# Performance work log

Hardware: AMD Instinct MI355X
Metric: run time of the kernel (lower is better)

Reference implementation:

```python
import jax, jax.numpy as jnp
import numpy as np

N, D, O, V, E, C = 100000, 128, 128, 3, 400000, 2

def setup_inputs() -> dict:
    key = jax.random.key(0)
    ks = jax.random.split(key, 32)
    s = 0.05
    inp = {
        'features': jax.random.normal(ks[0], (N, D), jnp.float32),
        'edge_index': jax.random.randint(ks[1], (V, 2, E), 0, N, jnp.int32),
        'edge_weight': jax.random.uniform(ks[2], (V, E), jnp.float32),
        # per-view RelationAggregator (single relation each)
        'rel_w': jax.random.normal(ks[3], (V, D, O)) * s,
        'rel_b': jnp.zeros((V, O)),
        'gate_w': jax.random.normal(ks[4], (V, O, O)) * s,
        'gate_b': jnp.zeros((V, O)),
        # LabelAwareAttention
        'la_w1': jax.random.normal(ks[5], (C, D, D // 2)) * s,
        'la_b1': jnp.zeros((C, D // 2)),
        'la_w2': jax.random.normal(ks[6], (C, D // 2)) * s,
        'la_b2': jnp.zeros((C,)),
        'pred_w': jax.random.normal(ks[7], (D, C)) * s,
        'pred_b': jnp.zeros((C,)),
        'att_bias': jnp.float32(0.1),
        # ViewLevelAttention
        'view_pref': jax.random.normal(ks[8], (V, O)),
        'va_w1': jax.random.normal(ks[9], (O, O // 2)) * s,
        'va_b1': jnp.zeros((O // 2,)),
        'va_w2': jax.random.normal(ks[10], (O // 2,)) * s,
        'va_b2': jnp.float32(0.0),
        # linear heads
        'ft_w': jax.random.normal(ks[11], (D, O)) * s,
        'ft_b': jnp.zeros((O,)),
        'sl_w': jax.random.normal(ks[12], (D, O)) * s,
        'sl_b': jnp.zeros((O,)),
        'fus_w': jax.random.normal(ks[13], (2 * O, O)) * s,
        'fus_b': jnp.zeros((O,)),
        'ln_g': jnp.ones((O,)),
        'ln_beta': jnp.zeros((O,)),
    }
    return inp


def _aggregate_view(features, ei, ew, w, b, gw, gb):
    # gather -> linear -> edge weight -> scatter-add (fused segment_sum)
    msg = (features[ei[0]] @ w + b) * ew[:, None]          # [E, O]
    agg = jax.ops.segment_sum(msg, ei[1], num_segments=N)  # [N, O]
    # relation_weight_net: softmax over 1 relation == 1.0 (identity)
    gate = jax.nn.sigmoid(agg @ gw + gb)
    return gate * agg


def reference(features, edge_index, edge_weight, rel_w, rel_b, gate_w, gate_b,
              la_w1, la_b1, la_w2, la_b2, pred_w, pred_b, att_bias,
              view_pref, va_w1, va_b1, va_w2, va_b2,
              ft_w, ft_b, sl_w, sl_b, fus_w, fus_b, ln_g, ln_beta):
    # --- label-aware attention ---
    class_probs = jax.nn.softmax(features @ pred_w + pred_b, axis=-1)        # [N, C]
    h = jax.nn.relu(jnp.einsum('nd,cdk->nck', features, la_w1) + la_b1)      # [N, C, D/2]
    scores = jax.nn.sigmoid(jnp.einsum('nck,ck->nc', h, la_w2) + la_b2)      # [N, C]
    node_att = jnp.sum(scores * class_probs, axis=-1) + att_bias             # [N]

    # --- per-view relation aggregation ---
    views = jax.vmap(_aggregate_view, in_axes=(None, 0, 0, 0, 0, 0, 0))(
        features, edge_index, edge_weight, rel_w, rel_b, gate_w, gate_b)     # [V, N, O]

    # --- view-level attention ---
    pe = views * view_pref[:, None, :]                                       # [V, N, O]
    vh = jax.nn.relu(jnp.einsum('vno,ok->vnk', pe, va_w1) + va_b1)           # [V, N, O/2]
    vscore = jnp.einsum('vnk,k->vn', vh, va_w2) + va_b2                      # [V, N]
    v_att = jax.nn.softmax(vscore, axis=0)                                   # over views
    combined = jnp.sum(views * v_att[..., None], axis=0)                     # [N, O]

    # --- fusion (dropout in eval mode == identity) ---
    self_out = features @ sl_w + sl_b
    transformed = features @ ft_w + ft_b
    weighted = combined * node_att[:, None]
    fused = jax.nn.relu(jnp.concatenate([self_out, weighted], axis=-1) @ fus_w + fus_b)
    out = fused + transformed

    mu = jnp.mean(out, axis=-1, keepdims=True)
    var = jnp.mean(jnp.square(out - mu), axis=-1, keepdims=True)
    out = (out - mu) / jnp.sqrt(var + 1e-5) * ln_g + ln_beta
    return out, class_probs
```

## Files before the change

### kernel.cpp

```cpp
#include <hip/hip_runtime.h>

#define N_ 100000
#define D_ 128
#define O_ 128
#define V_ 3
#define E_ 400000
#define NB_SCAN 98
#define EGRID 1563
#define MB 32
#define NBLK (N_ / MB)
#define LDA 136

#define PRE_CVT  6250
#define PRE_PREW (PRE_CVT + 64)
#define PRE_PREP (PRE_PREW + 683)
#define PRE_TOT  (PRE_PREP + 3 * EGRID)

typedef unsigned short u16;
typedef __attribute__((ext_vector_type(8))) short bf16x8;
typedef __attribute__((ext_vector_type(4))) float f32x4;

#define MFMA16x16x32 __builtin_amdgcn_mfma_f32_16x16x32_bf16

#define P_RELB  0
#define P_GATEB 384
#define P_VP    768
#define P_VAB1  1152
#define P_VAW2  1216
#define P_VAB2  1280
#define P_LAB1  1281
#define P_LAW2  1409
#define P_LAB2  1537
#define P_PREDB 1539
#define P_ATTB  1541
#define P_FTB   1542
#define P_LNG   1670
#define P_LNB   1798
#define P_PREDW 1926
#define P_TOTAL 2182

__device__ __forceinline__ float b2f(u16 u) {
    union { float f; unsigned int i; } x; x.i = ((unsigned int)u) << 16; return x.f;
}
__device__ __forceinline__ float blo(unsigned int u) {
    union { float f; unsigned int i; } x; x.i = u << 16; return x.f;
}
__device__ __forceinline__ float bhi(unsigned int u) {
    union { float f; unsigned int i; } x; x.i = u & 0xffff0000u; return x.f;
}
__device__ __forceinline__ u16 f2b(float f) {
    union { float f; unsigned int i; } x; x.f = f;
    unsigned int r = x.i + 0x7FFFu + ((x.i >> 16) & 1u);
    return (u16)(r >> 16);
}

template<int F32> __device__ __forceinline__ float LD(const void* p, size_t i) {
    if (F32) return ((const float*)p)[i];
    return b2f(((const u16*)p)[i]);
}

__global__ void k_detect(const u16* __restrict__ feat, int* __restrict__ flag) {
    int t = threadIdx.x;
    u16 a = feat[2 * t], b = feat[2 * t + 128];
    int zeros = (a == 0 ? 1 : 0) + (b == 0 ? 1 : 0);
    float va = b2f(a), vb = b2f(b);
    int bad = (!(va > -128.f && va < 128.f) ? 1 : 0) +
              (!(vb > -128.f && vb < 128.f) ? 1 : 0);
    #pragma unroll
    for (int s = 1; s <= 32; s <<= 1) {
        bad += __shfl_xor(bad, s);
        zeros += __shfl_xor(zeros, s);
    }
    if (t == 0) flag[0] = (bad >= 16 || zeros >= 64) ? 1 : 0;
}

__device__ __forceinline__ void cvt_body_f32(int b, const void* feat,
                                             u16* __restrict__ featB) {
    size_t idx = (size_t)b * 256 + threadIdx.x;
    const float4* fp = (const float4*)feat;
    float4 a = fp[idx * 2], c = fp[idx * 2 + 1];
    uint4 u;
    u.x = (unsigned)f2b(a.x) | ((unsigned)f2b(a.y) << 16);
    u.y = (unsigned)f2b(a.z) | ((unsigned)f2b(a.w) << 16);
    u.z = (unsigned)f2b(c.x) | ((unsigned)f2b(c.y) << 16);
    u.w = (unsigned)f2b(c.z) | ((unsigned)f2b(c.w) << 16);
    ((uint4*)featB)[idx] = u;
}

template<int F32>
__device__ __forceinline__ void prew_body(int b, const void* sl_w, const void* sl_b,
                                          const void* fus_w, const void* fus_b,
                                          u16* __restrict__ W1T, float* __restrict__ b1) {
    int gid = b * 256 + threadIdx.x;
    int d = gid >> 7, o = gid & 127;
    float acc = 0.f;
    for (int k = 0; k < 128; ++k)
        acc += LD<F32>(sl_w, d * 128 + k) * LD<F32>(fus_w, k * 128 + o);
    W1T[o * 128 + d] = f2b(acc);
    if (gid < 128) {
        float accb = 0.f;
        for (int k = 0; k < 128; ++k)
            accb += LD<F32>(sl_b, k) * LD<F32>(fus_w, k * 128 + gid);
        b1[gid] = accb + LD<F32>(fus_b, gid);
    }
}

template<int F32>
__device__ __forceinline__ void prep_body(int b,
        const void* rel_w, const void* gate_w, const void* va_w1, const void* fus_w,
        const void* ft_w, const void* la_w1,
        const void* rel_b, const void* gate_b, const void* vpref,
        const void* va_b1, const void* va_w2, const void* va_b2,
        const void* la_b1, const void* la_w2, const void* la_b2,
        const void* pred_b, const void* att_bias, const void* ft_b,
        const void* ln_g, const void* ln_beta, const void* pred_w,
        u16* __restrict__ relT, u16* __restrict__ rgT, u16* __restrict__ vaT3,
        u16* __restrict__ fus2T, u16* __restrict__ ftT, u16* __restrict__ laT,
        float* __restrict__ P, float* __restrict__ rgb) {
    int id = b * 256 + threadIdx.x;
    if (id < 49152) {
        int v = id >> 14, r = id & 16383, o = r >> 7, d = r & 127;
        relT[id] = f2b(LD<F32>(rel_w, (size_t)v * 16384 + d * 128 + o));
    } else if (id < 73728) {
        int t = id - 49152, v = t >> 13, r = t & 8191, n = r >> 7, k = r & 127;
        vaT3[t] = f2b(LD<F32>(va_w1, k * 64 + n) * LD<F32>(vpref, v * 128 + k));
    } else if (id < 90112) {
        int t = id - 73728, n = t >> 7, k = t & 127;
        fus2T[t] = f2b(LD<F32>(fus_w, (128 + k) * 128 + n));
    } else if (id < 106496) {
        int t = id - 90112, o = t >> 7, d = t & 127;
        ftT[t] = f2b(LD<F32>(ft_w, d * 128 + o));
    } else if (id < 122880) {
        int t = id - 106496, n = t >> 7, d = t & 127;
        int c = n >> 6, j = n & 63;
        laT[t] = f2b(LD<F32>(la_w1, c * 8192 + d * 64 + j));
    } else if (id < 122880 + P_TOTAL) {
        int t = id - 122880;
        float val;
        if      (t < P_GATEB) val = LD<F32>(rel_b, t);
        else if (t < P_VP)    val = LD<F32>(gate_b, t - P_GATEB);
        else if (t < P_VAB1)  val = LD<F32>(vpref, t - P_VP);
        else if (t < P_VAW2)  val = LD<F32>(va_b1, t - P_VAB1);
        else if (t < P_VAB2)  val = LD<F32>(va_w2, t - P_VAW2);
        else if (t < P_LAB1)  val = LD<F32>(va_b2, 0);
        else if (t < P_LAW2)  val = LD<F32>(la_b1, t - P_LAB1);
        else if (t < P_LAB2)  val = LD<F32>(la_w2, t - P_LAW2);
        else if (t < P_PREDB) val = LD<F32>(la_b2, t - P_LAB2);
        else if (t < P_ATTB)  val = LD<F32>(pred_b, t - P_PREDB);
        else if (t < P_FTB)   val = LD<F32>(att_bias, 0);
        else if (t < P_LNG)   val = LD<F32>(ft_b, t - P_FTB);
        else if (t < P_LNB)   val = LD<F32>(ln_g, t - P_LNG);
        else if (t < P_PREDW) val = LD<F32>(ln_beta, t - P_LNB);
        else                  val = LD<F32>(pred_w, t - P_PREDW);
        P[t] = val;
    } else if (id < 174214) {
        int t = id - 125062, v = t >> 14, r = t & 16383, n = r >> 7, d = r & 127;
        float acc = 0.f;
        for (int o = 0; o < 128; ++o)
            acc += LD<F32>(rel_w,  (size_t)v * 16384 + d * 128 + o) *
                   LD<F32>(gate_w, (size_t)v * 16384 + o * 128 + n);
        rgT[t] = f2b(acc);
    } else if (id < 174598) {
        int t = id - 174214, v = t >> 7, n = t & 127;
        float acc = 0.f;
        for (int o = 0; o < 128; ++o)
            acc += LD<F32>(rel_b, v * 128 + o) *
                   LD<F32>(gate_w, (size_t)v * 16384 + o * 128 + n);
        rgb[t] = acc;
    }
}

__global__ __launch_bounds__(256) void k_preC(const int* __restrict__ flag,
        const void* feat, u16* __restrict__ featB,
        const void* sl_w, const void* sl_b, const void* fus_w, const void* fus_b,
        u16* __restrict__ W1T, float* __restrict__ b1,
        const void* rel_w, const void* gate_w, const void* va_w1,
        const void* ft_w, const void* la_w1,
        const void* rel_b, const void* gate_b, const void* vpref,
        const void* va_b1, const void* va_w2, const void* va_b2,
        const void* la_b1, const void* la_w2, const void* la_b2,
        const void* pred_b, const void* att_bias, const void* ft_b,
        const void* ln_g, const void* ln_beta, const void* pred_w,
        u16* __restrict__ relT, u16* __restrict__ rgT, u16* __restrict__ vaT3,
        u16* __restrict__ fus2T, u16* __restrict__ ftT, u16* __restrict__ laT,
        float* __restrict__ P, float* __restrict__ rgb,
        const int* __restrict__ ei, int* __restrict__ cur3) {
    int b = blockIdx.x;
    if (b < PRE_CVT) {
        if (flag[0]) cvt_body_f32(b, feat, featB);
    } else if (b < PRE_PREW) {
        if (flag[0]) prew_body<1>(b - PRE_CVT, sl_w, sl_b, fus_w, fus_b, W1T, b1);
        else         prew_body<0>(b - PRE_CVT, sl_w, sl_b, fus_w, fus_b, W1T, b1);
    } else if (b < PRE_PREP) {
        if (flag[0]) prep_body<1>(b - PRE_PREW, rel_w, gate_w, va_w1, fus_w, ft_w, la_w1,
                                  rel_b, gate_b, vpref, va_b1, va_w2, va_b2,
                                  la_b1, la_w2, la_b2, pred_b, att_bias, ft_b,
                                  ln_g, ln_beta, pred_w, relT, rgT, vaT3, fus2T, ftT, laT, P, rgb);
        else         prep_body<0>(b - PRE_PREW, rel_w, gate_w, va_w1, fus_w, ft_w, la_w1,
                                  rel_b, gate_b, vpref, va_b1, va_w2, va_b2,
                                  la_b1, la_w2, la_b2, pred_b, att_bias, ft_b,
                                  ln_g, ln_beta, pred_w, relT, rgT, vaT3, fus2T, ftT, laT, P, rgb);
    } else {
        int b2 = b - PRE_PREP;
        int v = b2 / EGRID;
        int e = (b2 % EGRID) * 256 + threadIdx.x;
        if (e < E_) atomicAdd(&cur3[v * N_ + ei[(size_t)v * 2 * E_ + E_ + e]], 1);
    }
}

__global__ __launch_bounds__(256) void k_scan_bsum(const int* __restrict__ cur3,
                                                   int* __restrict__ bsum) {
    __shared__ int red[256];
    const int v = blockIdx.x / NB_SCAN, b = blockIdx.x % NB_SCAN, tid = threadIdx.x;
    const int base = b * 1024;
    const int* counts = cur3 + v * N_;
    int s = 0;
    for (int i = tid; i < 1024; i += 256) {
        int idx = base + i;
        s += (idx < N_) ? counts[idx] : 0;
    }
    red[tid] = s;
    __syncthreads();
    for (int st = 128; st >= 1; st >>= 1) {
        if (tid < st) red[tid] += red[tid + st];
        __syncthreads();
    }
    if (tid == 0) bsum[v * 128 + b] = red[0];
}

__global__ __launch_bounds__(256) void k_scan_write(int* __restrict__ cur3,
                                                    const int* __restrict__ bsum,
                                                    int* __restrict__ offs3) {
    __shared__ int lsum[256];
    __shared__ int bs_s[128];
    const int v = blockIdx.x / NB_SCAN, b = blockIdx.x % NB_SCAN, tid = threadIdx.x;
    const int base = b * 1024;
    int* counts = cur3 + v * N_;
    int* offs   = offs3 + v * N_;
    if (tid < 128) bs_s[tid] = (tid < b) ? bsum[v * 128 + tid] : 0;
    int c[4]; int s = 0;
    #pragma unroll
    for (int k = 0; k < 4; ++k) {
        int idx = base + tid * 4 + k;
        c[k] = (idx < N_) ? counts[idx] : 0;
        s += c[k];
    }
    lsum[tid] = s;
    __syncthreads();
    for (int st = 1; st < 256; st <<= 1) {
        int t = (tid >= st) ? lsum[tid - st] : 0;
        __syncthreads();
        lsum[tid] += t;
        __syncthreads();
    }
    for (int st = 64; st >= 1; st >>= 1) {
        if (tid < st) bs_s[tid] += bs_s[tid + st];
        __syncthreads();
    }
    int off = bs_s[0] + lsum[tid] - s;
    #pragma unroll
    for (int k = 0; k < 4; ++k) {
        int idx = base + tid * 4 + k;
        if (idx < N_) { offs[idx] = off; counts[idx] = off; }
        off += c[k];
    }
}

template<int F32>
__device__ __forceinline__ void place_body(const int* __restrict__ ei, const void* ew_all,
                                           int* __restrict__ cur3, int2* __restrict__ srcw3) {
    int v = blockIdx.x / EGRID;
    int e = (blockIdx.x % EGRID) * 256 + threadIdx.x;
    if (e < E_) {
        int dst = ei[(size_t)v * 2 * E_ + E_ + e];
        int src = ei[(size_t)v * 2 * E_ + e];
        float w = LD<F32>(ew_all, (size_t)v * E_ + e);
        int pos = atomicAdd(&cur3[v * N_ + dst], 1);
        int2 sw; sw.x = src; sw.y = __float_as_int(w);
        srcw3[(size_t)v * E_ + pos] = sw;
    }
}
__global__ __launch_bounds__(256) void k_place(const int* __restrict__ flag,
                                               const int* __restrict__ ei, const void* ew,
                                               int* __restrict__ cur3, int2* __restrict__ srcw3) {
    if (flag[0]) place_body<1>(ei, ew, cur3, srcw3);
    else         place_body<0>(ei, ew, cur3, srcw3);
}

__global__ __launch_bounds__(768, 6) void k_fused(const int* __restrict__ flag,
        const void* feat, const u16* __restrict__ featB_,
        const int2* __restrict__ srcw3,
        const int* __restrict__ offs3, const int* __restrict__ ends3,
        const u16* __restrict__ relT, const u16* __restrict__ rgT,
        const u16* __restrict__ vaT3, const u16* __restrict__ W1T,
        const u16* __restrict__ fus2T, const u16* __restrict__ ftT,
        const u16* __restrict__ laT,
        const float* __restrict__ b1, const float* __restrict__ rgb,
        const float* __restrict__ P,
        void* __restrict__ d_out) {
    const int f32 = flag[0];
    const u16* __restrict__ fb = f32 ? featB_ : (const u16*)feat;

    __shared__ __align__(16) u16 S[4 * MB * LDA];
    __shared__ float redL[4][MB];
    __shared__ float redv[3][4][MB];
    __shared__ float wsn3[3][MB];
    __shared__ float aw_s[MB][3];
    __shared__ float natt_s[MB];
    __shared__ float lg_s[MB][2];
    __shared__ float mrs_s[MB][2];

    u16* xA = S;
    float* F1 = (float*)(S + 2 * MB * LDA);
    float* F2 = (float*)S;
    float* red2 = &redv[0][0][0];

    const int tid = threadIdx.x;
    const int g   = tid >> 8;
    const int t256 = tid & 255;
    const int wid = t256 >> 6;
    const int L = t256 & 63, q = L >> 4, i = L & 15;
    const int nb = wid * 32;
    const int nodebase = blockIdx.x * MB;
    const int nl = t256 >> 5, l32 = t256 & 31, o4 = l32 * 4;
    const int gsub = t256 >> 4, l16 = tid & 15, o8 = l16 * 8;
    const f32x4 zz = {0.f, 0.f, 0.f, 0.f};
    u16* zc = S + (size_t)(1 + g) * MB * LDA;

    auto ldf = [&](const u16* B, int row, int k0) -> bf16x8 {
        return *(const bf16x8*)&B[row * LDA + k0];
    };
    auto ldg = [&](const u16* B, int row, int k0) -> bf16x8 {
        return *(const bf16x8*)&B[row * 128 + k0];
    };
    auto gemm32 = [&](const u16* A, const u16* Bg, f32x4 acc[2][2]) {
        #pragma unroll
        for (int kk = 0; kk < 4; ++kk) {
            int k0 = q * 8 + kk * 32;
            bf16x8 a0 = ldf(A, i, k0);
            bf16x8 a1 = ldf(A, i + 16, k0);
            bf16x8 bb0 = ldg(Bg, nb + i, k0);
            bf16x8 bb1 = ldg(Bg, nb + 16 + i, k0);
            acc[0][0] = MFMA16x16x32(a0, bb0, acc[0][0], 0, 0, 0);
            acc[0][1] = MFMA16x16x32(a0, bb1, acc[0][1], 0, 0, 0);
            acc[1][0] = MFMA16x16x32(a1, bb0, acc[1][0], 0, 0, 0);
            acc[1][1] = MFMA16x16x32(a1, bb1, acc[1][1], 0, 0, 0);
        }
    };
    auto gemm32x2 = [&](const u16* A, const u16* B0g, const u16* B1g,
                        f32x4 accA[2][2], f32x4 accB[2][2]) {
        #pragma unroll
        for (int kk = 0; kk < 4; ++kk) {
            int k0 = q * 8 + kk * 32;
            bf16x8 a0 = ldf(A, i, k0);
            bf16x8 a1 = ldf(A, i + 16, k0);
            bf16x8 p0 = ldg(B0g, nb + i, k0);
            bf16x8 p1 = ldg(B0g, nb + 16 + i, k0);
            bf16x8 r0 = ldg(B1g, nb + i, k0);
            bf16x8 r1 = ldg(B1g, nb + 16 + i, k0);
            accA[0][0] = MFMA16x16x32(a0, p0, accA[0][0], 0, 0, 0);
            accA[0][1] = MFMA16x16x32(a0, p1, accA[0][1], 0, 0, 0);
            accA[1][0] = MFMA16x16x32(a1, p0, accA[1][0], 0, 0, 0);
            accA[1][1] = MFMA16x16x32(a1, p1, accA[1][1], 0, 0, 0);
            accB[0][0] = MFMA16x16x32(a0, r0, accB[0][0], 0, 0, 0);
            accB[0][1] = MFMA16x16x32(a0, r1, accB[0][1], 0, 0, 0);
            accB[1][0] = MFMA16x16x32(a1, r0, accB[1][0], 0, 0, 0);
            accB[1][1] = MFMA16x16x32(a1, r1, accB[1][1], 0, 0, 0);
        }
    };
    auto gather = [&]() {
        const int* offs = offs3 + g * N_;
        const int* ends = ends3 + g * N_;
        const int2* srcw = srcw3 + (size_t)g * E_;
        #pragma unroll
        for (int rep = 0; rep < 2; ++rep) {
            const int m = gsub + rep * 16;
            const int node = nodebase + m;
            float z0 = 0.f, z1 = 0.f, z2 = 0.f, z3 = 0.f;
            float z4 = 0.f, z5 = 0.f, z6 = 0.f, z7 = 0.f, ws = 0.f;
            int j = offs[node], jend = ends[node];
            while (j < jend) {
                int r = jend - j;
                int2 e0 = srcw[j];
                int2 e1, e2, e3;
                e1.x = 0; e1.y = 0; e2.x = 0; e2.y = 0; e3.x = 0; e3.y = 0;
                if (r > 1) e1 = srcw[j + 1];
                if (r > 2) e2 = srcw[j + 2];
                if (r > 3) e3 = srcw[j + 3];
                uint4 x0, x1, x2, x3;
                x1.x = x1.y = x1.z = x1.w = 0;
                x2.x = x2.y = x2.z = x2.w = 0;
                x3.x = x3.y = x3.z = x3.w = 0;
                x0 = *(const uint4*)&fb[(size_t)e0.x * 128 + o8];
                if (r > 1) x1 = *(const uint4*)&fb[(size_t)e1.x * 128 + o8];
                if (r > 2) x2 = *(const uint4*)&fb[(size_t)e2.x * 128 + o8];
                if (r > 3) x3 = *(const uint4*)&fb[(size_t)e3.x * 128 + o8];
                float w0 = __int_as_float(e0.y), w1 = __int_as_float(e1.y);
                float w2 = __int_as_float(e2.y), w3 = __int_as_float(e3.y);
                ws += w0 + w1 + w2 + w3;
                z0 += w0 * blo(x0.x) + w1 * blo(x1.x) + w2 * blo(x2.x) + w3 * blo(x3.x);
                z1 += w0 * bhi(x0.x) + w1 * bhi(x1.x) + w2 * bhi(x2.x) + w3 * bhi(x3.x);
                z2 += w0 * blo(x0.y) + w1 * blo(x1.y) + w2 * blo(x2.y) + w3 * blo(x3.y);
                z3 += w0 * bhi(x0.y) + w1 * bhi(x1.y) + w2 * bhi(x2.y) + w3 * bhi(x3.y);
                z4 += w0 * blo(x0.z) + w1 * blo(x1.z) + w2 * blo(x2.z) + w3 * blo(x3.z);
                z5 += w0 * bhi(x0.z) + w1 * bhi(x1.z) + w2 * bhi(x2.z) + w3 * bhi(x3.z);
                z6 += w0 * blo(x0.w) + w1 * blo(x1.w) + w2 * blo(x2.w) + w3 * blo(x3.w);
                z7 += w0 * bhi(x0.w) + w1 * bhi(x1.w) + w2 * bhi(x2.w) + w3 * bhi(x3.w);
                j += 4;
            }
            uint4 u;
            u.x = (unsigned)f2b(z0) | ((unsigned)f2b(z1) << 16);
            u.y = (unsigned)f2b(z2) | ((unsigned)f2b(z3) << 16);
            u.z = (unsigned)f2b(z4) | ((unsigned)f2b(z5) << 16);
            u.w = (unsigned)f2b(z6) | ((unsigned)f2b(z7) << 16);
            *(uint4*)&zc[m * LDA + o8] = u;
            if (l16 == 0) wsn3[g][m] = ws;
        }
    };

    if (tid < 512) {
        int m = tid >> 4, s = tid & 15;
        *(uint4*)&xA[m * LDA + s * 8] =
            *(const uint4*)&fb[(size_t)(nodebase + m) * 128 + s * 8];
    }
    gather();
    __syncthreads();

    if (g == 1) {
        f32x4 accL[2][2] = {{zz, zz}, {zz, zz}};
        gemm32(xA, laT, accL);
        float la0 = P[P_LAB1 + nb + i],  la1 = P[P_LAB1 + nb + 16 + i];
        float lw0 = P[P_LAW2 + nb + i],  lw1 = P[P_LAW2 + nb + 16 + i];
        float partL[2][4];
        #pragma unroll
        for (int mt = 0; mt < 2; ++mt)
            #pragma unroll
            for (int r = 0; r < 4; ++r) {
                float h0 = fmaxf(accL[mt][0][r] + la0, 0.f);
                float h1 = fmaxf(accL[mt][1][r] + la1, 0.f);
                partL[mt][r] = h0 * lw0 + h1 * lw1;
            }
        #pragma unroll
        for (int s = 1; s <= 8; s <<= 1)
            #pragma unroll
            for (int mt = 0; mt < 2; ++mt)
                #pragma unroll
                for (int r = 0; r < 4; ++r)
                    partL[mt][r] += __shfl_xor(partL[mt][r], s);
        if (i == 0)
            #pragma unroll
            for (int mt = 0; mt < 2; ++mt)
                #pragma unroll
                for (int r = 0; r < 4; ++r)
                    redL[wid][mt * 16 + q * 4 + r] = partL[mt][r];
    }
    if (g == 2) {
        float pw[8];
        #pragma unroll
        for (int t = 0; t < 4; ++t) {
            pw[2 * t]     = P[P_PREDW + (o4 + t) * 2];
            pw[2 * t + 1] = P[P_PREDW + (o4 + t) * 2 + 1];
        }
        #pragma unroll
        for (int rep = 0; rep < 4; ++rep) {
            int m = rep * 8 + nl;
            float lg0 = 0.f, lg1 = 0.f;
            #pragma unroll
            for (int t = 0; t < 4; ++t) {
                float xv = b2f(xA[m * LDA + o4 + t]);
                lg0 += xv * pw[2 * t];
                lg1 += xv * pw[2 * t + 1];
            }
            #pragma unroll
            for (int s = 1; s <= 16; s <<= 1) {
                lg0 += __shfl_xor(lg0, s);
                lg1 += __shfl_xor(lg1, s);
            }
            if (l32 == 0) { lg_s[m][0] = lg0; lg_s[m][1] = lg1; }
        }
    }
    f32x4 accA[2][2] = {{zz, zz}, {zz, zz}};
    f32x4 accG[2][2] = {{zz, zz}, {zz, zz}};
    gemm32x2(zc, relT + (size_t)g * 16384, rgT + (size_t)g * 16384, accA, accG);
    __syncthreads();

    {
        float rb0 = P[P_RELB + g * 128 + nb + i];
        float rb1 = P[P_RELB + g * 128 + nb + 16 + i];
        float rg0 = rgb[g * 128 + nb + i];
        float rg1 = rgb[g * 128 + nb + 16 + i];
        float gb0 = P[P_GATEB + g * 128 + nb + i];
        float gb1 = P[P_GATEB + g * 128 + nb + 16 + i];
        #pragma unroll
        for (int mt = 0; mt < 2; ++mt)
            #pragma unroll
            for (int nt = 0; nt < 2; ++nt) {
                float rb = nt ? rb1 : rb0;
                float rg = nt ? rg1 : rg0;
                float gb = nt ? gb1 : gb0;
                int col = nb + nt * 16 + i;
                #pragma unroll
                for (int r = 0; r < 4; ++r) {
                    int row = mt * 16 + q * 4 + r;
                    float ws = wsn3[g][row];
                    float agg = accA[mt][nt][r] + ws * rb;
                    float gin = accG[mt][nt][r] + ws * rg + gb;
                    float gt = 1.f / (1.f + __expf(-gin));
                    zc[row * LDA + col] = f2b(gt * agg);
                }
            }
    }
    if (tid < MB) {
        float c0 = redL[0][tid] + redL[1][tid] + P[P_LAB2 + 0];
        float c1 = redL[2][tid] + redL[3][tid] + P[P_LAB2 + 1];
        float s0 = 1.f / (1.f + __expf(-c0));
        float s1 = 1.f / (1.f + __expf(-c1));
        float l0 = lg_s[tid][0] + P[P_PREDB + 0];
        float l1 = lg_s[tid][1] + P[P_PREDB + 1];
        float mx = fmaxf(l0, l1);
        float e0 = __expf(l0 - mx), e1 = __expf(l1 - mx);
        float inv = 1.f / (e0 + e1);
        float p0 = e0 * inv, p1 = e1 * inv;
        natt_s[tid] = s0 * p0 + s1 * p1 + P[P_ATTB];
        int node = nodebase + tid;
        if (f32) {
            float* pr = (float*)d_out + (size_t)N_ * O_;
            pr[node * 2 + 0] = p0; pr[node * 2 + 1] = p1;
        } else {
            u16* pr = (u16*)d_out + (size_t)N_ * O_;
            pr[node * 2 + 0] = f2b(p0); pr[node * 2 + 1] = f2b(p1);
        }
    }
    __syncthreads();

    {
        f32x4 accV[2] = {zz, zz};
        const int nbv = wid * 16, colv = nbv + i;
        const u16* vaW = vaT3 + (size_t)g * 8192;
        #pragma unroll
        for (int kk = 0; kk < 4; ++kk) {
            int k0 = q * 8 + kk * 32;
            bf16x8 bb = ldg(vaW, nbv + i, k0);
            bf16x8 a0 = ldf(zc, i, k0);
            bf16x8 a1 = ldf(zc, i + 16, k0);
            accV[0] = MFMA16x16x32(a0, bb, accV[0], 0, 0, 0);
            accV[1] = MFMA16x16x32(a1, bb, accV[1], 0, 0, 0);
        }
        float vb1v = P[P_VAB1 + colv], vw2v = P[P_VAW2 + colv];
        float part[2][4];
        #pragma unroll
        for (int mt = 0; mt < 2; ++mt)
            #pragma unroll
            for (int r = 0; r < 4; ++r) {
                float vh = fmaxf(accV[mt][r] + vb1v, 0.f);
                part[mt][r] = vh * vw2v;
            }
        #pragma unroll
        for (int s = 1; s <= 8; s <<= 1)
            #pragma unroll
            for (int mt = 0; mt < 2; ++mt)
                #pragma unroll
                for (int r = 0; r < 4; ++r)
                    part[mt][r] += __shfl_xor(part[mt][r], s);
        if (i == 0)
            #pragma unroll
            for (int mt = 0; mt < 2; ++mt)
                #pragma unroll
                for (int r = 0; r < 4; ++r)
                    redv[g][wid][mt * 16 + q * 4 + r] = part[mt][r];
    }
    __syncthreads();

    if (tid < MB) {
        float sv[3];
        #pragma unroll
        for (int v = 0; v < 3; ++v)
            sv[v] = redv[v][0][tid] + redv[v][1][tid] +
                    redv[v][2][tid] + redv[v][3][tid] + P[P_VAB2];
        float mx = fmaxf(sv[0], fmaxf(sv[1], sv[2]));
        float e0 = __expf(sv[0] - mx), e1 = __expf(sv[1] - mx), e2 = __expf(sv[2] - mx);
        float inv = natt_s[tid] / (e0 + e1 + e2);
        aw_s[tid][0] = e0 * inv; aw_s[tid][1] = e1 * inv; aw_s[tid][2] = e2 * inv;
    }
    __syncthreads();

    {
        u16* z0p = S + MB * LDA;
        u16* z1p = S + 2 * MB * LDA;
        u16* z2p = S + 3 * MB * LDA;
        for (int idx = tid; idx < MB * 128; idx += 768) {
            int row = idx >> 7, col = idx & 127;
            float w = aw_s[row][0] * b2f(z0p[row * LDA + col]) +
                      aw_s[row][1] * b2f(z1p[row * LDA + col]) +
                      aw_s[row][2] * b2f(z2p[row * LDA + col]);
            z0p[row * LDA + col] = f2b(w);
        }
    }
    __syncthreads();

    f32x4 accF[2][2] = {{zz, zz}, {zz, zz}};
    if (g == 0) {
        gemm32(xA, W1T, accF);
        #pragma unroll
        for (int mt = 0; mt < 2; ++mt)
            #pragma unroll
            for (int nt = 0; nt < 2; ++nt)
                #pragma unroll
                for (int r = 0; r < 4; ++r)
                    F1[(mt * 16 + q * 4 + r) * 128 + nb + nt * 16 + i] = accF[mt][nt][r];
    } else if (g == 1) {
        gemm32(S + MB * LDA, fus2T, accF);
    } else {
        gemm32(xA, ftT, accF);
    }
    __syncthreads();
    if (g == 1) {
        #pragma unroll
        for (int mt = 0; mt < 2; ++mt)
            #pragma unroll
            for (int nt = 0; nt < 2; ++nt)
                #pragma unroll
                for (int r = 0; r < 4; ++r)
                    F2[(mt * 16 + q * 4 + r) * 128 + nb + nt * 16 + i] = accF[mt][nt][r];
    }
    __syncthreads();

    if (g == 2) {
        float b1v0 = b1[nb + i], b1v1 = b1[nb + 16 + i];
        float fb0 = P[P_FTB + nb + i], fb1 = P[P_FTB + nb + 16 + i];
        float ps[2][4], pq[2][4];
        #pragma unroll
        for (int mt = 0; mt < 2; ++mt)
            #pragma unroll
            for (int r = 0; r < 4; ++r) { ps[mt][r] = 0.f; pq[mt][r] = 0.f; }
        #pragma unroll
        for (int mt = 0; mt < 2; ++mt)
            #pragma unroll
            for (int nt = 0; nt < 2; ++nt) {
                int col = nb + nt * 16 + i;
                float bv = nt ? b1v1 : b1v0;
                float fv = nt ? fb1 : fb0;
                #pragma unroll
                for (int r = 0; r < 4; ++r) {
                    int rc = (mt * 16 + q * 4 + r) * 128 + col;
                    float o = fmaxf(F1[rc] + F2[rc] + bv, 0.f) + accF[mt][nt][r] + fv;
                    F1[rc] = o;
                    ps[mt][r] += o; pq[mt][r] += o * o;
                }
            }
        #pragma unroll
        for (int s = 1; s <= 8; s <<= 1)
            #pragma unroll
            for (int mt = 0; mt < 2; ++mt)
                #pragma unroll
                for (int r = 0; r < 4; ++r) {
                    ps[mt][r] += __shfl_xor(ps[mt][r], s);
                    pq[mt][r] += __shfl_xor(pq[mt][r], s);
                }
        if (i == 0)
            #pragma unroll
            for (int mt = 0; mt < 2; ++mt)
                #pragma unroll
                for (int r = 0; r < 4; ++r) {
                    int row = mt * 16 + q * 4 + r;
                    red2[(wid * MB + row) * 2 + 0] = ps[mt][r];
                    red2[(wid * MB + row) * 2 + 1] = pq[mt][r];
                }
    }
    __syncthreads();

    if (tid < MB) {
        float sm = red2[tid * 2]            + red2[(MB + tid) * 2] +
                   red2[(2 * MB + tid) * 2] + red2[(3 * MB + tid) * 2];
        float sq = red2[tid * 2 + 1]            + red2[(MB + tid) * 2 + 1] +
                   red2[(2 * MB + tid) * 2 + 1] + red2[(3 * MB + tid) * 2 + 1];
        float mu = sm * (1.f / 128.f);
        float var = sq * (1.f / 128.f) - mu * mu;
        mrs_s[tid][0] = mu; mrs_s[tid][1] = rsqrtf(var + 1e-5f);
    }
    __syncthreads();

    if (f32) {
        float* op = (float*)d_out + (size_t)nodebase * 128;
        for (int idx = tid; idx < MB * 128; idx += 768) {
            int row = idx >> 7, col = idx & 127;
            op[idx] = (F1[idx] - mrs_s[row][0]) * mrs_s[row][1]
                      * P[P_LNG + col] + P[P_LNB + col];
        }
    } else {
        unsigned* op = (unsigned*)d_out + (size_t)nodebase * 64;
        for (int idx = tid; idx < MB * 64; idx += 768) {
            int row = idx >> 6, c2 = (idx & 63) * 2;
            float m0 = mrs_s[row][0], r0 = mrs_s[row][1];
            float v0 = (F1[row * 128 + c2]     - m0) * r0 * P[P_LNG + c2]     + P[P_LNB + c2];
            float v1 = (F1[row * 128 + c2 + 1] - m0) * r0 * P[P_LNG + c2 + 1] + P[P_LNB + c2 + 1];
            op[idx] = (unsigned)f2b(v0) | ((unsigned)f2b(v1) << 16);
        }
    }
}

extern "C" void kernel_launch(void* const* d_in, const int* in_sizes, int n_in,
                              void* d_out, int out_size, void* d_ws, size_t ws_size,
                              hipStream_t stream) {
    const void* feat     = d_in[0];
    const int*  ei       = (const int*)d_in[1];
    const void* ew       = d_in[2];
    const void* rel_w    = d_in[3];
    const void* rel_b    = d_in[4];
    const void* gate_w   = d_in[5];
    const void* gate_b   = d_in[6];
    const void* la_w1    = d_in[7];
    const void* la_b1    = d_in[8];
    const void* la_w2    = d_in[9];
    const void* la_b2    = d_in[10];
    const void* pred_w   = d_in[11];
    const void* pred_b   = d_in[12];
    const void* att_bias = d_in[13];
    const void* view_pref= d_in[14];
    const void* va_w1    = d_in[15];
    const void* va_b1    = d_in[16];
    const void* va_w2    = d_in[17];
    const void* va_b2    = d_in[18];
    const void* ft_w     = d_in[19];
    const void* ft_b     = d_in[20];
    const void* sl_w     = d_in[21];
    const void* sl_b     = d_in[22];
    const void* fus_w    = d_in[23];
    const void* fus_b    = d_in[24];
    const void* ln_g     = d_in[25];
    const void* ln_beta  = d_in[26];

    int*   flag  = (int*)d_ws;
    int*   offs3 = flag + 4;
    int*   cur3  = offs3 + 3 * N_;
    int2*  srcw3 = (int2*)(cur3 + 3 * N_);
    int*   bsum  = (int*)(srcw3 + 3 * E_);
    float* b1    = (float*)(bsum + 3 * 128);
    float* P     = b1 + 128;
    float* rgb   = P + 2304;
    u16*   W1T   = (u16*)(rgb + 384);
    u16*   relT  = W1T + 16384;
    u16*   rgT   = relT + 3 * 16384;
    u16*   vaT3  = rgT + 3 * 16384;
    u16*   fus2T = vaT3 + 3 * 8192;
    u16*   ftT   = fus2T + 16384;
    u16*   laT   = ftT + 16384;
    u16*   featB = laT + 16384;

    k_detect<<<1, 64, 0, stream>>>((const u16*)feat, flag);
    (void)hipMemsetAsync(cur3, 0, 3 * N_ * sizeof(int), stream);
    k_preC<<<PRE_TOT, 256, 0, stream>>>(flag, feat, featB,
                                        sl_w, sl_b, fus_w, fus_b, W1T, b1,
                                        rel_w, gate_w, va_w1, ft_w, la_w1,
                                        rel_b, gate_b, view_pref,
                                        va_b1, va_w2, va_b2,
                                        la_b1, la_w2, la_b2,
                                        pred_b, att_bias, ft_b, ln_g, ln_beta, pred_w,
                                        relT, rgT, vaT3, fus2T, ftT, laT, P, rgb,
                                        ei, cur3);
    k_scan_bsum<<<3 * NB_SCAN, 256, 0, stream>>>(cur3, bsum);
    k_scan_write<<<3 * NB_SCAN, 256, 0, stream>>>(cur3, bsum, offs3);
    k_place<<<3 * EGRID, 256, 0, stream>>>(flag, ei, ew, cur3, srcw3);
    k_fused<<<NBLK, 768, 0, stream>>>(flag, feat, featB, srcw3, offs3, cur3,
                                      relT, rgT, vaT3, W1T, fus2T, ftT, laT,
                                      b1, rgb, P, d_out);
}
```

Measured before the change: 517.5 us.

## Inline dtype detection per kernel, drop barriers, and raise MFMA wave priority

Removes the separate single-block detect kernel and instead has each kernel infer the input dtype from the feature bits in every wavefront, cutting one launch and the flag dependency. In the fused kernel, the per-row attention weights and layernorm statistics are now recomputed inline by every thread, which removes two __syncthreads and the shared staging arrays at the cost of redundant exp and reduction arithmetic. MFMA loops are wrapped in s_setprio to favour matrix waves. Every wave now performs extra global reads and shuffles for detection.

```diff
diff --git a/kernel.cpp b/kernel.cpp
--- a/kernel.cpp
+++ b/kernel.cpp
@@ -59,9 +59,10 @@
     return b2f(((const u16*)p)[i]);
 }
 
-__global__ void k_detect(const u16* __restrict__ feat, int* __restrict__ flag) {
-    int t = threadIdx.x;
-    u16 a = feat[2 * t], b = feat[2 * t + 128];
+__device__ __forceinline__ int detect_f32(const void* feat) {
+    const u16* f = (const u16*)feat;
+    int l = threadIdx.x & 63;
+    u16 a = f[2 * l], b = f[2 * l + 128];
     int zeros = (a == 0 ? 1 : 0) + (b == 0 ? 1 : 0);
     float va = b2f(a), vb = b2f(b);
     int bad = (!(va > -128.f && va < 128.f) ? 1 : 0) +
@@ -71,7 +72,7 @@
         bad += __shfl_xor(bad, s);
         zeros += __shfl_xor(zeros, s);
     }
-    if (t == 0) flag[0] = (bad >= 16 || zeros >= 64) ? 1 : 0;
+    return (bad >= 16 || zeros >= 64) ? 1 : 0;
 }
 
 __device__ __forceinline__ void cvt_body_f32(int b, const void* feat,
@@ -170,7 +171,7 @@
     }
 }
 
-__global__ __launch_bounds__(256) void k_preC(const int* __restrict__ flag,
+__global__ __launch_bounds__(256) void k_preC(
         const void* feat, u16* __restrict__ featB,
         const void* sl_w, const void* sl_b, const void* fus_w, const void* fus_b,
         u16* __restrict__ W1T, float* __restrict__ b1,
@@ -185,21 +186,22 @@
         u16* __restrict__ fus2T, u16* __restrict__ ftT, u16* __restrict__ laT,
         float* __restrict__ P, float* __restrict__ rgb,
         const int* __restrict__ ei, int* __restrict__ cur3) {
+    const int f32 = detect_f32(feat);
     int b = blockIdx.x;
     if (b < PRE_CVT) {
-        if (flag[0]) cvt_body_f32(b, feat, featB);
+        if (f32) cvt_body_f32(b, feat, featB);
     } else if (b < PRE_PREW) {
-        if (flag[0]) prew_body<1>(b - PRE_CVT, sl_w, sl_b, fus_w, fus_b, W1T, b1);
-        else         prew_body<0>(b - PRE_CVT, sl_w, sl_b, fus_w, fus_b, W1T, b1);
+        if (f32) prew_body<1>(b - PRE_CVT, sl_w, sl_b, fus_w, fus_b, W1T, b1);
+        else     prew_body<0>(b - PRE_CVT, sl_w, sl_b, fus_w, fus_b, W1T, b1);
     } else if (b < PRE_PREP) {
-        if (flag[0]) prep_body<1>(b - PRE_PREW, rel_w, gate_w, va_w1, fus_w, ft_w, la_w1,
-                                  rel_b, gate_b, vpref, va_b1, va_w2, va_b2,
-                                  la_b1, la_w2, la_b2, pred_b, att_bias, ft_b,
-                                  ln_g, ln_beta, pred_w, relT, rgT, vaT3, fus2T, ftT, laT, P, rgb);
-        else         prep_body<0>(b - PRE_PREW, rel_w, gate_w, va_w1, fus_w, ft_w, la_w1,
-                                  rel_b, gate_b, vpref, va_b1, va_w2, va_b2,
-                                  la_b1, la_w2, la_b2, pred_b, att_bias, ft_b,
-                                  ln_g, ln_beta, pred_w, relT, rgT, vaT3, fus2T, ftT, laT, P, rgb);
+        if (f32) prep_body<1>(b - PRE_PREW, rel_w, gate_w, va_w1, fus_w, ft_w, la_w1,
+                              rel_b, gate_b, vpref, va_b1, va_w2, va_b2,
+                              la_b1, la_w2, la_b2, pred_b, att_bias, ft_b,
+                              ln_g, ln_beta, pred_w, relT, rgT, vaT3, fus2T, ftT, laT, P, rgb);
+        else     prep_body<0>(b - PRE_PREW, rel_w, gate_w, va_w1, fus_w, ft_w, la_w1,
+                              rel_b, gate_b, vpref, va_b1, va_w2, va_b2,
+                              la_b1, la_w2, la_b2, pred_b, att_bias, ft_b,
+                              ln_g, ln_beta, pred_w, relT, rgT, vaT3, fus2T, ftT, laT, P, rgb);
     } else {
         int b2 = b - PRE_PREP;
         int v = b2 / EGRID;
@@ -280,14 +282,14 @@
         srcw3[(size_t)v * E_ + pos] = sw;
     }
 }
-__global__ __launch_bounds__(256) void k_place(const int* __restrict__ flag,
+__global__ __launch_bounds__(256) void k_place(const void* feat,
                                                const int* __restrict__ ei, const void* ew,
                                                int* __restrict__ cur3, int2* __restrict__ srcw3) {
-    if (flag[0]) place_body<1>(ei, ew, cur3, srcw3);
-    else         place_body<0>(ei, ew, cur3, srcw3);
-}
-
-__global__ __launch_bounds__(768, 6) void k_fused(const int* __restrict__ flag,
+    if (detect_f32(feat)) place_body<1>(ei, ew, cur3, srcw3);
+    else                  place_body<0>(ei, ew, cur3, srcw3);
+}
+
+__global__ __launch_bounds__(768, 6) void k_fused(
         const void* feat, const u16* __restrict__ featB_,
         const int2* __restrict__ srcw3,
         const int* __restrict__ offs3, const int* __restrict__ ends3,
@@ -298,17 +300,14 @@
         const float* __restrict__ b1, const float* __restrict__ rgb,
         const float* __restrict__ P,
         void* __restrict__ d_out) {
-    const int f32 = flag[0];
+    const int f32 = detect_f32(feat);
     const u16* __restrict__ fb = f32 ? featB_ : (const u16*)feat;
 
     __shared__ __align__(16) u16 S[4 * MB * LDA];
     __shared__ float redL[4][MB];
     __shared__ float redv[3][4][MB];
     __shared__ float wsn3[3][MB];
-    __shared__ float aw_s[MB][3];
-    __shared__ float natt_s[MB];
     __shared__ float lg_s[MB][2];
-    __shared__ float mrs_s[MB][2];
 
     u16* xA = S;
     float* F1 = (float*)(S + 2 * MB * LDA);
@@ -334,6 +333,7 @@
         return *(const bf16x8*)&B[row * 128 + k0];
     };
     auto gemm32 = [&](const u16* A, const u16* Bg, f32x4 acc[2][2]) {
+        __builtin_amdgcn_s_setprio(1);
         #pragma unroll
         for (int kk = 0; kk < 4; ++kk) {
             int k0 = q * 8 + kk * 32;
@@ -346,9 +346,11 @@
             acc[1][0] = MFMA16x16x32(a1, bb0, acc[1][0], 0, 0, 0);
             acc[1][1] = MFMA16x16x32(a1, bb1, acc[1][1], 0, 0, 0);
         }
+        __builtin_amdgcn_s_setprio(0);
     };
     auto gemm32x2 = [&](const u16* A, const u16* B0g, const u16* B1g,
                         f32x4 accA[2][2], f32x4 accB[2][2]) {
+        __builtin_amdgcn_s_setprio(1);
         #pragma unroll
         for (int kk = 0; kk < 4; ++kk) {
             int k0 = q * 8 + kk * 32;
@@ -367,6 +369,7 @@
             accB[1][0] = MFMA16x16x32(a1, r0, accB[1][0], 0, 0, 0);
             accB[1][1] = MFMA16x16x32(a1, r1, accB[1][1], 0, 0, 0);
         }
+        __builtin_amdgcn_s_setprio(0);
     };
     auto gather = [&]() {
         const int* offs = offs3 + g * N_;
@@ -511,17 +514,12 @@
             }
     }
     if (tid < MB) {
-        float c0 = redL[0][tid] + redL[1][tid] + P[P_LAB2 + 0];
-        float c1 = redL[2][tid] + redL[3][tid] + P[P_LAB2 + 1];
-        float s0 = 1.f / (1.f + __expf(-c0));
-        float s1 = 1.f / (1.f + __expf(-c1));
         float l0 = lg_s[tid][0] + P[P_PREDB + 0];
         float l1 = lg_s[tid][1] + P[P_PREDB + 1];
         float mx = fmaxf(l0, l1);
         float e0 = __expf(l0 - mx), e1 = __expf(l1 - mx);
         float inv = 1.f / (e0 + e1);
         float p0 = e0 * inv, p1 = e1 * inv;
-        natt_s[tid] = s0 * p0 + s1 * p1 + P[P_ATTB];
         int node = nodebase + tid;
         if (f32) {
             float* pr = (float*)d_out + (size_t)N_ * O_;
@@ -537,6 +535,7 @@
         f32x4 accV[2] = {zz, zz};
         const int nbv = wid * 16, colv = nbv + i;
         const u16* vaW = vaT3 + (size_t)g * 8192;
+        __builtin_amdgcn_s_setprio(1);
         #pragma unroll
         for (int kk = 0; kk < 4; ++kk) {
             int k0 = q * 8 + kk * 32;
@@ -546,6 +545,7 @@
             accV[0] = MFMA16x16x32(a0, bb, accV[0], 0, 0, 0);
             accV[1] = MFMA16x16x32(a1, bb, accV[1], 0, 0, 0);
         }
+        __builtin_amdgcn_s_setprio(0);
         float vb1v = P[P_VAB1 + colv], vw2v = P[P_VAW2 + colv];
         float part[2][4];
         #pragma unroll
@@ -571,28 +571,33 @@
     }
     __syncthreads();
 
-    if (tid < MB) {
-        float sv[3];
-        #pragma unroll
-        for (int v = 0; v < 3; ++v)
-            sv[v] = redv[v][0][tid] + redv[v][1][tid] +
-                    redv[v][2][tid] + redv[v][3][tid] + P[P_VAB2];
-        float mx = fmaxf(sv[0], fmaxf(sv[1], sv[2]));
-        float e0 = __expf(sv[0] - mx), e1 = __expf(sv[1] - mx), e2 = __expf(sv[2] - mx);
-        float inv = natt_s[tid] / (e0 + e1 + e2);
-        aw_s[tid][0] = e0 * inv; aw_s[tid][1] = e1 * inv; aw_s[tid][2] = e2 * inv;
-    }
-    __syncthreads();
-
     {
         u16* z0p = S + MB * LDA;
         u16* z1p = S + 2 * MB * LDA;
         u16* z2p = S + 3 * MB * LDA;
+        float vab2 = P[P_VAB2], attb = P[P_ATTB];
+        float lab20 = P[P_LAB2 + 0], lab21 = P[P_LAB2 + 1];
+        float pb0 = P[P_PREDB + 0], pb1 = P[P_PREDB + 1];
         for (int idx = tid; idx < MB * 128; idx += 768) {
             int row = idx >> 7, col = idx & 127;
-            float w = aw_s[row][0] * b2f(z0p[row * LDA + col]) +
-                      aw_s[row][1] * b2f(z1p[row * LDA + col]) +
-                      aw_s[row][2] * b2f(z2p[row * LDA + col]);
+            float c0 = redL[0][row] + redL[1][row] + lab20;
+            float c1 = redL[2][row] + redL[3][row] + lab21;
+            float s0 = 1.f / (1.f + __expf(-c0));
+            float s1 = 1.f / (1.f + __expf(-c1));
+            float l0 = lg_s[row][0] + pb0;
+            float l1 = lg_s[row][1] + pb1;
+            float mx2 = fmaxf(l0, l1);
+            float q0 = __expf(l0 - mx2), q1 = __expf(l1 - mx2);
+            float natt = (s0 * q0 + s1 * q1) / (q0 + q1) + attb;
+            float sv0 = redv[0][0][row] + redv[0][1][row] + redv[0][2][row] + redv[0][3][row] + vab2;
+            float sv1 = redv[1][0][row] + redv[1][1][row] + redv[1][2][row] + redv[1][3][row] + vab2;
+            float sv2 = redv[2][0][row] + redv[2][1][row] + redv[2][2][row] + redv[2][3][row] + vab2;
+            float mx = fmaxf(sv0, fmaxf(sv1, sv2));
+            float e0 = __expf(sv0 - mx), e1 = __expf(sv1 - mx), e2 = __expf(sv2 - mx);
+            float inv = natt / (e0 + e1 + e2);
+            float w = (e0 * b2f(z0p[row * LDA + col]) +
+                       e1 * b2f(z1p[row * LDA + col]) +
+                       e2 * b2f(z2p[row * LDA + col])) * inv;
             z0p[row * LDA + col] = f2b(w);
         }
     }
@@ -669,31 +674,30 @@
     }
     __syncthreads();
 
-    if (tid < MB) {
-        float sm = red2[tid * 2]            + red2[(MB + tid) * 2] +
-                   red2[(2 * MB + tid) * 2] + red2[(3 * MB + tid) * 2];
-        float sq = red2[tid * 2 + 1]            + red2[(MB + tid) * 2 + 1] +
-                   red2[(2 * MB + tid) * 2 + 1] + red2[(3 * MB + tid) * 2 + 1];
-        float mu = sm * (1.f / 128.f);
-        float var = sq * (1.f / 128.f) - mu * mu;
-        mrs_s[tid][0] = mu; mrs_s[tid][1] = rsqrtf(var + 1e-5f);
-    }
-    __syncthreads();
-
     if (f32) {
         float* op = (float*)d_out + (size_t)nodebase * 128;
         for (int idx = tid; idx < MB * 128; idx += 768) {
             int row = idx >> 7, col = idx & 127;
-            op[idx] = (F1[idx] - mrs_s[row][0]) * mrs_s[row][1]
-                      * P[P_LNG + col] + P[P_LNB + col];
+            float sm = red2[row * 2]              + red2[(MB + row) * 2] +
+                       red2[(2 * MB + row) * 2]   + red2[(3 * MB + row) * 2];
+            float sq = red2[row * 2 + 1]            + red2[(MB + row) * 2 + 1] +
+                       red2[(2 * MB + row) * 2 + 1] + red2[(3 * MB + row) * 2 + 1];
+            float mu = sm * (1.f / 128.f);
+            float rs = rsqrtf(sq * (1.f / 128.f) - mu * mu + 1e-5f);
+            op[idx] = (F1[idx] - mu) * rs * P[P_LNG + col] + P[P_LNB + col];
         }
     } else {
         unsigned* op = (unsigned*)d_out + (size_t)nodebase * 64;
         for (int idx = tid; idx < MB * 64; idx += 768) {
             int row = idx >> 6, c2 = (idx & 63) * 2;
-            float m0 = mrs_s[row][0], r0 = mrs_s[row][1];
-            float v0 = (F1[row * 128 + c2]     - m0) * r0 * P[P_LNG + c2]     + P[P_LNB + c2];
-            float v1 = (F1[row * 128 + c2 + 1] - m0) * r0 * P[P_LNG + c2 + 1] + P[P_LNB + c2 + 1];
+            float sm = red2[row * 2]              + red2[(MB + row) * 2] +
+                       red2[(2 * MB + row) * 2]   + red2[(3 * MB + row) * 2];
+            float sq = red2[row * 2 + 1]            + red2[(MB + row) * 2 + 1] +
+                       red2[(2 * MB + row) * 2 + 1] + red2[(3 * MB + row) * 2 + 1];
+            float mu = sm * (1.f / 128.f);
+            float rs = rsqrtf(sq * (1.f / 128.f) - mu * mu + 1e-5f);
+            float v0 = (F1[row * 128 + c2]     - mu) * rs * P[P_LNG + c2]     + P[P_LNB + c2];
+            float v1 = (F1[row * 128 + c2 + 1] - mu) * rs * P[P_LNG + c2 + 1] + P[P_LNB + c2 + 1];
             op[idx] = (unsigned)f2b(v0) | ((unsigned)f2b(v1) << 16);
         }
     }
@@ -747,9 +751,8 @@
     u16*   laT   = ftT + 16384;
     u16*   featB = laT + 16384;
 
-    k_detect<<<1, 64, 0, stream>>>((const u16*)feat, flag);
     (void)hipMemsetAsync(cur3, 0, 3 * N_ * sizeof(int), stream);
-    k_preC<<<PRE_TOT, 256, 0, stream>>>(flag, feat, featB,
+    k_preC<<<PRE_TOT, 256, 0, stream>>>(feat, featB,
                                         sl_w, sl_b, fus_w, fus_b, W1T, b1,
                                         rel_w, gate_w, va_w1, ft_w, la_w1,
                                         rel_b, gate_b, view_pref,
@@ -760,8 +763,8 @@
                                         ei, cur3);
     k_scan_bsum<<<3 * NB_SCAN, 256, 0, stream>>>(cur3, bsum);
     k_scan_write<<<3 * NB_SCAN, 256, 0, stream>>>(cur3, bsum, offs3);
-    k_place<<<3 * EGRID, 256, 0, stream>>>(flag, ei, ew, cur3, srcw3);
-    k_fused<<<NBLK, 768, 0, stream>>>(flag, feat, featB, srcw3, offs3, cur3,
+    k_place<<<3 * EGRID, 256, 0, stream>>>(feat, ei, ew, cur3, srcw3);
+    k_fused<<<NBLK, 768, 0, stream>>>(feat, featB, srcw3, offs3, cur3,
                                       relT, rgT, vaT3, W1T, fus2T, ftT, laT,
                                       b1, rgb, P, d_out);
 }
```

Result: slower. 571.6 us (+10.4%).

## Merge scan kernels, derive CSR starts from counts, drop a fused-kernel barrier

Applied to the files above, without the earlier changes.

Replaces the two-pass block-sum scan with a single kernel where each block sums all preceding counts directly, which removes one launch and the bsum buffer. The placement atomics now advance offs3 in place, so offs3 ends up holding each segment's end and the count array stays intact. The gather derives each segment's start as end minus count. In the fused kernel, the fus2 GEMM result goes into a dedicated shared buffer, which removes one __syncthreads and the extra write phase at the cost of 16KB more LDS per block. That extra LDS may lower occupancy, and the redundant prefix reads grow quadratically with the number of blocks.

```diff
diff --git a/kernel.cpp b/kernel.cpp
--- a/kernel.cpp
+++ b/kernel.cpp
@@ -208,36 +208,24 @@
     }
 }
 
-__global__ __launch_bounds__(256) void k_scan_bsum(const int* __restrict__ cur3,
-                                                   int* __restrict__ bsum) {
+__global__ __launch_bounds__(256) void k_scan_write(const int* __restrict__ cur3,
+                                                    int* __restrict__ offs3) {
     __shared__ int red[256];
+    __shared__ int lsum[256];
+    __shared__ int bs;
     const int v = blockIdx.x / NB_SCAN, b = blockIdx.x % NB_SCAN, tid = threadIdx.x;
     const int base = b * 1024;
     const int* counts = cur3 + v * N_;
-    int s = 0;
-    for (int i = tid; i < 1024; i += 256) {
-        int idx = base + i;
-        s += (idx < N_) ? counts[idx] : 0;
-    }
-    red[tid] = s;
+    int* offs = offs3 + v * N_;
+    int pre = 0;
+    for (int idx = tid; idx < base; idx += 256) pre += counts[idx];
+    red[tid] = pre;
     __syncthreads();
     for (int st = 128; st >= 1; st >>= 1) {
         if (tid < st) red[tid] += red[tid + st];
         __syncthreads();
     }
-    if (tid == 0) bsum[v * 128 + b] = red[0];
-}
-
-__global__ __launch_bounds__(256) void k_scan_write(int* __restrict__ cur3,
-                                                    const int* __restrict__ bsum,
-                                                    int* __restrict__ offs3) {
-    __shared__ int lsum[256];
-    __shared__ int bs_s[128];
-    const int v = blockIdx.x / NB_SCAN, b = blockIdx.x % NB_SCAN, tid = threadIdx.x;
-    const int base = b * 1024;
-    int* counts = cur3 + v * N_;
-    int* offs   = offs3 + v * N_;
-    if (tid < 128) bs_s[tid] = (tid < b) ? bsum[v * 128 + tid] : 0;
+    if (tid == 0) bs = red[0];
     int c[4]; int s = 0;
     #pragma unroll
     for (int k = 0; k < 4; ++k) {
@@ -253,44 +241,40 @@
         lsum[tid] += t;
         __syncthreads();
     }
-    for (int st = 64; st >= 1; st >>= 1) {
-        if (tid < st) bs_s[tid] += bs_s[tid + st];
-        __syncthreads();
-    }
-    int off = bs_s[0] + lsum[tid] - s;
+    int off = bs + lsum[tid] - s;
     #pragma unroll
     for (int k = 0; k < 4; ++k) {
         int idx = base + tid * 4 + k;
-        if (idx < N_) { offs[idx] = off; counts[idx] = off; }
+        if (idx < N_) offs[idx] = off;
         off += c[k];
     }
 }
 
 template<int F32>
 __device__ __forceinline__ void place_body(const int* __restrict__ ei, const void* ew_all,
-                                           int* __restrict__ cur3, int2* __restrict__ srcw3) {
+                                           int* __restrict__ offs3, int2* __restrict__ srcw3) {
     int v = blockIdx.x / EGRID;
     int e = (blockIdx.x % EGRID) * 256 + threadIdx.x;
     if (e < E_) {
         int dst = ei[(size_t)v * 2 * E_ + E_ + e];
         int src = ei[(size_t)v * 2 * E_ + e];
         float w = LD<F32>(ew_all, (size_t)v * E_ + e);
-        int pos = atomicAdd(&cur3[v * N_ + dst], 1);
+        int pos = atomicAdd(&offs3[v * N_ + dst], 1);
         int2 sw; sw.x = src; sw.y = __float_as_int(w);
         srcw3[(size_t)v * E_ + pos] = sw;
     }
 }
 __global__ __launch_bounds__(256) void k_place(const int* __restrict__ flag,
                                                const int* __restrict__ ei, const void* ew,
-                                               int* __restrict__ cur3, int2* __restrict__ srcw3) {
-    if (flag[0]) place_body<1>(ei, ew, cur3, srcw3);
-    else         place_body<0>(ei, ew, cur3, srcw3);
+                                               int* __restrict__ offs3, int2* __restrict__ srcw3) {
+    if (flag[0]) place_body<1>(ei, ew, offs3, srcw3);
+    else         place_body<0>(ei, ew, offs3, srcw3);
 }
 
 __global__ __launch_bounds__(768, 6) void k_fused(const int* __restrict__ flag,
         const void* feat, const u16* __restrict__ featB_,
         const int2* __restrict__ srcw3,
-        const int* __restrict__ offs3, const int* __restrict__ ends3,
+        const int* __restrict__ ends3, const int* __restrict__ counts3,
         const u16* __restrict__ relT, const u16* __restrict__ rgT,
         const u16* __restrict__ vaT3, const u16* __restrict__ W1T,
         const u16* __restrict__ fus2T, const u16* __restrict__ ftT,
@@ -302,6 +286,7 @@
     const u16* __restrict__ fb = f32 ? featB_ : (const u16*)feat;
 
     __shared__ __align__(16) u16 S[4 * MB * LDA];
+    __shared__ __align__(16) float F2d[MB * 128];
     __shared__ float redL[4][MB];
     __shared__ float redv[3][4][MB];
     __shared__ float wsn3[3][MB];
@@ -312,7 +297,6 @@
 
     u16* xA = S;
     float* F1 = (float*)(S + 2 * MB * LDA);
-    float* F2 = (float*)S;
     float* red2 = &redv[0][0][0];
 
     const int tid = threadIdx.x;
@@ -369,8 +353,8 @@
         }
     };
     auto gather = [&]() {
-        const int* offs = offs3 + g * N_;
         const int* ends = ends3 + g * N_;
+        const int* cnts = counts3 + g * N_;
         const int2* srcw = srcw3 + (size_t)g * E_;
         #pragma unroll
         for (int rep = 0; rep < 2; ++rep) {
@@ -378,7 +362,8 @@
             const int node = nodebase + m;
             float z0 = 0.f, z1 = 0.f, z2 = 0.f, z3 = 0.f;
             float z4 = 0.f, z5 = 0.f, z6 = 0.f, z7 = 0.f, ws = 0.f;
-            int j = offs[node], jend = ends[node];
+            int jend = ends[node];
+            int j = jend - cnts[node];
             while (j < jend) {
                 int r = jend - j;
                 int2 e0 = srcw[j];
@@ -610,18 +595,15 @@
                     F1[(mt * 16 + q * 4 + r) * 128 + nb + nt * 16 + i] = accF[mt][nt][r];
     } else if (g == 1) {
         gemm32(S + MB * LDA, fus2T, accF);
+        #pragma unroll
+        for (int mt = 0; mt < 2; ++mt)
+            #pragma unroll
+            for (int nt = 0; nt < 2; ++nt)
+                #pragma unroll
+                for (int r = 0; r < 4; ++r)
+                    F2d[(mt * 16 + q * 4 + r) * 128 + nb + nt * 16 + i] = accF[mt][nt][r];
     } else {
         gemm32(xA, ftT, accF);
-    }
-    __syncthreads();
-    if (g == 1) {
-        #pragma unroll
-        for (int mt = 0; mt < 2; ++mt)
-            #pragma unroll
-            for (int nt = 0; nt < 2; ++nt)
-                #pragma unroll
-                for (int r = 0; r < 4; ++r)
-                    F2[(mt * 16 + q * 4 + r) * 128 + nb + nt * 16 + i] = accF[mt][nt][r];
     }
     __syncthreads();
 
@@ -643,7 +625,7 @@
                 #pragma unroll
                 for (int r = 0; r < 4; ++r) {
                     int rc = (mt * 16 + q * 4 + r) * 128 + col;
-                    float o = fmaxf(F1[rc] + F2[rc] + bv, 0.f) + accF[mt][nt][r] + fv;
+                    float o = fmaxf(F1[rc] + F2d[rc] + bv, 0.f) + accF[mt][nt][r] + fv;
                     F1[rc] = o;
                     ps[mt][r] += o; pq[mt][r] += o * o;
                 }
@@ -758,9 +740,8 @@
                                         pred_b, att_bias, ft_b, ln_g, ln_beta, pred_w,
                                         relT, rgT, vaT3, fus2T, ftT, laT, P, rgb,
                                         ei, cur3);
-    k_scan_bsum<<<3 * NB_SCAN, 256, 0, stream>>>(cur3, bsum);
-    k_scan_write<<<3 * NB_SCAN, 256, 0, stream>>>(cur3, bsum, offs3);
-    k_place<<<3 * EGRID, 256, 0, stream>>>(flag, ei, ew, cur3, srcw3);
+    k_scan_write<<<3 * NB_SCAN, 256, 0, stream>>>(cur3, offs3);
+    k_place<<<3 * EGRID, 256, 0, stream>>>(flag, ei, ew, offs3, srcw3);
     k_fused<<<NBLK, 768, 0, stream>>>(flag, feat, featB, srcw3, offs3, cur3,
                                       relT, rgT, vaT3, W1T, fus2T, ftT, laT,
                                       b1, rgb, P, d_out);
```

Result: slower. 567.3 us (+9.6%).
